# Kernel tuning notes

Hardware: AMD Instinct MI355X
Metric: run time of the kernel (lower is better)

The kernel has to match this reference:

```python
import jax, jax.numpy as jnp
import numpy as np

B, S, D = 4, 2048, 512
H, DK, DV = 8, 64, 64
EPS = 1e-6
MASK_FILL = -1e-9  # faithful to the original masked_fill value (NOT -inf)


def setup_inputs() -> dict:
    key = jax.random.key(0)
    ks = jax.random.split(key, 9)
    sc = 0.05
    return {
        "q": jax.random.normal(ks[0], (B, S, D), jnp.float32),
        "k": jax.random.normal(ks[1], (B, S, D), jnp.float32),
        "v": jax.random.normal(ks[2], (B, S, D), jnp.float32),
        "src_mask": jax.random.randint(ks[3], (B, S), 0, 2, jnp.int32),
        "Wq": jax.random.normal(ks[4], (D, H * DK), jnp.float32) * sc,
        "Wk": jax.random.normal(ks[5], (D, H * DK), jnp.float32) * sc,
        "Wv": jax.random.normal(ks[6], (D, H * DV), jnp.float32) * sc,
        "Wo": jax.random.normal(ks[7], (H * DV, D), jnp.float32) * sc,
        "gamma": jnp.ones((D,), jnp.float32),
        "beta": jnp.zeros((D,), jnp.float32),
    }


def reference(q, k, v, src_mask, Wq, Wk, Wv, Wo, gamma, beta):
    b, len_q, _ = q.shape
    residual = q
    # QKV projections -> [B, H, S, dk/dv]
    qh = (q @ Wq).reshape(b, len_q, H, DK).transpose(0, 2, 1, 3)
    kh = (k @ Wk).reshape(b, -1, H, DK).transpose(0, 2, 1, 3)
    vh = (v @ Wv).reshape(b, -1, H, DV).transpose(0, 2, 1, 3)
    # scores [B, H, S, S]
    attn = jnp.einsum('bhqd,bhkd->bhqk', qh, kh) / jnp.sqrt(jnp.float32(DK))
    # pairwise src mask: outer product of [B,S] mask, diagonal forced to 1
    sm = src_mask[:, :len_q].astype(jnp.float32)
    am = sm[:, :, None] * sm[:, None, :]               # [B, S, S]
    idx = jnp.arange(len_q)
    am = am.at[:, idx, idx].set(1.0)
    attn = jnp.where(am[:, None, :, :] == 0, MASK_FILL, attn)
    attn = jax.nn.softmax(attn, axis=-1)
    out = jnp.einsum('bhqk,bhkd->bhqd', attn, vh)      # [B, H, S, dv]
    out = out.transpose(0, 2, 1, 3).reshape(b, len_q, H * DV)
    out = out @ Wo + residual
    # LayerNorm(eps=1e-6)
    mu = jnp.mean(out, axis=-1, keepdims=True)
    var = jnp.var(out, axis=-1, keepdims=True)
    out = (out - mu) * jax.lax.rsqrt(var + EPS) * gamma + beta
    return out, attn
```

## Files before the change

### kernel.cpp

```cpp
#include <hip/hip_runtime.h>
#include <math.h>

#define B_ 4
#define S_ 2048
#define D_ 512
#define H_ 8
#define NEG_FILL (-1e-9f)

typedef __attribute__((ext_vector_type(8))) short bf16x8;
typedef __attribute__((ext_vector_type(4))) float f32x4;

#define MFMA16(A, Bm, C) __builtin_amdgcn_mfma_f32_16x16x32_bf16((A), (Bm), (C), 0, 0, 0)

__device__ __forceinline__ short f2b(float f) {
  union { float f; unsigned u; } x;
  x.f = f;
  unsigned r = x.u + 0x7fffu + ((x.u >> 16) & 1u);
  return (short)(r >> 16);
}

__global__ __launch_bounds__(256) void prep_wt(
    const float* __restrict__ Wq, const float* __restrict__ Wk,
    const float* __restrict__ Wv, const float* __restrict__ Wo,
    short* __restrict__ Wqt, short* __restrict__ Wkt,
    short* __restrict__ Wvt, short* __restrict__ Wot)
{
  const float* W; short* Wt;
  switch (blockIdx.z) {
    case 0: W = Wq; Wt = Wqt; break;
    case 1: W = Wk; Wt = Wkt; break;
    case 2: W = Wv; Wt = Wvt; break;
    default: W = Wo; Wt = Wot; break;
  }
  __shared__ float Ws[64 * 68];
  const int t = threadIdx.x;
  const int n0 = blockIdx.x * 64, k0 = blockIdx.y * 64;

  #pragma unroll
  for (int rep = 0; rep < 4; ++rep) {
    int e4 = rep * 256 + t;
    int r = e4 >> 4, c0 = (e4 & 15) * 4;
    *(float4*)&Ws[r * 68 + c0] = *(const float4*)&W[(size_t)(k0 + r) * 512 + n0 + c0];
  }
  __syncthreads();

  int rn = t >> 2;
  int kb = (t & 3) * 16;
  union { short s[8]; int4 v; } pk;
  #pragma unroll
  for (int half = 0; half < 2; ++half) {
    #pragma unroll
    for (int i = 0; i < 8; ++i)
      pk.s[i] = f2b(Ws[(kb + half * 8 + i) * 68 + rn]);
    *(int4*)&Wt[(size_t)(n0 + rn) * 512 + k0 + kb + half * 8] = pk.v;
  }
}

__global__ __launch_bounds__(256) void x2b(
    const float* __restrict__ q, const float* __restrict__ k, const float* __restrict__ v,
    short* __restrict__ qb, short* __restrict__ kb, short* __restrict__ vb)
{
  const float* X = (blockIdx.y == 0) ? q : (blockIdx.y == 1) ? k : v;
  short* Y = (blockIdx.y == 0) ? qb : (blockIdx.y == 1) ? kb : vb;
  const size_t i = ((size_t)blockIdx.x * 256 + threadIdx.x) * 8;
  float4 a = *(const float4*)&X[i];
  float4 b = *(const float4*)&X[i + 4];
  union { short s[8]; int4 v; } pk;
  pk.s[0] = f2b(a.x); pk.s[1] = f2b(a.y); pk.s[2] = f2b(a.z); pk.s[3] = f2b(a.w);
  pk.s[4] = f2b(b.x); pk.s[5] = f2b(b.y); pk.s[6] = f2b(b.z); pk.s[7] = f2b(b.w);
  *(int4*)&Y[i] = pk.v;
}

__global__ __launch_bounds__(256) void qkv_mfma(
    const short* __restrict__ qb, const short* __restrict__ kb, const short* __restrict__ vb,
    const short* __restrict__ Wqt, const short* __restrict__ Wkt, const short* __restrict__ Wvt,
    short* __restrict__ qh, short* __restrict__ kh, short* __restrict__ vt)
{
  const int z = blockIdx.z;
  const short* Xb = (z == 0) ? qb : (z == 1) ? kb : vb;
  const short* Wt = (z == 0) ? Wqt : (z == 1) ? Wkt : Wvt;

  __shared__ short Xs[64 * 72];
  __shared__ short Wsh[64 * 72];

  const int t = threadIdx.x;
  const int wave = t >> 6, lane = t & 63, quad = lane >> 4, l15 = lane & 15;
  const int tile_n = blockIdx.x * 64;
  const int tile_m = blockIdx.y * 64;

  f32x4 acc[4];
  #pragma unroll
  for (int nt = 0; nt < 4; ++nt) acc[nt] = (f32x4){0.f, 0.f, 0.f, 0.f};

  for (int k0 = 0; k0 < 512; k0 += 64) {
    __syncthreads();
    #pragma unroll
    for (int rep = 0; rep < 2; ++rep) {
      int e = rep * 256 + t;
      int row = e >> 3, c0 = (e & 7) * 8;
      *(int4*)&Xs[row * 72 + c0] = *(const int4*)&Xb[(size_t)(tile_m + row) * 512 + k0 + c0];
      *(int4*)&Wsh[row * 72 + c0] = *(const int4*)&Wt[(size_t)(tile_n + row) * 512 + k0 + c0];
    }
    __syncthreads();
    #pragma unroll
    for (int ks = 0; ks < 2; ++ks) {
      bf16x8 af = *(bf16x8*)&Xs[(wave * 16 + l15) * 72 + ks * 32 + quad * 8];
      #pragma unroll
      for (int nt = 0; nt < 4; ++nt) {
        bf16x8 bfr = *(bf16x8*)&Wsh[(nt * 16 + l15) * 72 + ks * 32 + quad * 8];
        acc[nt] = MFMA16(af, bfr, acc[nt]);
      }
    }
  }

  const int h = tile_n >> 6;
  if (z < 2) {
    short* Y = (z == 0) ? qh : kh;
    #pragma unroll
    for (int nt = 0; nt < 4; ++nt) {
      int d = nt * 16 + l15;
      #pragma unroll
      for (int r = 0; r < 4; ++r) {
        int row = tile_m + wave * 16 + quad * 4 + r;
        int b = row >> 11, s = row & (S_ - 1);
        Y[(((size_t)(b * H_ + h)) * S_ + s) * 64 + d] = f2b(acc[nt][r]);
      }
    }
  } else {
    int row0 = tile_m + wave * 16 + quad * 4;
    int b = row0 >> 11, s0 = row0 & (S_ - 1);
    #pragma unroll
    for (int nt = 0; nt < 4; ++nt) {
      int d = nt * 16 + l15;
      short4 pk = make_short4(f2b(acc[nt][0]), f2b(acc[nt][1]),
                              f2b(acc[nt][2]), f2b(acc[nt][3]));
      *(short4*)&vt[(((size_t)(b * H_ + h)) * 64 + d) * S_ + s0] = pk;
    }
  }
}

__global__ __launch_bounds__(256) void attn_mfma(
    const short* __restrict__ qh, const short* __restrict__ kh,
    const short* __restrict__ vt, const int* __restrict__ src_mask,
    float* __restrict__ attn_out, short* __restrict__ ohb)
{
  const int t = threadIdx.x;
  const int wave = t >> 6, lane = t & 63, quad = lane >> 4, l15 = lane & 15;

  const int lin = blockIdx.y * 32 + blockIdx.x;
  const int nl  = (lin & 7) * 128 + (lin >> 3);
  const int bh = nl >> 5, b = bh >> 3, h = bh & 7;
  const int q0 = (nl & 31) * 64;

  __shared__ __align__(16) short KV[4][64 * 64];
  __shared__ __align__(16) short Ps[4][16 * 72];
  __shared__ __align__(16) int smAll[S_];

  const short* __restrict__ khb = kh + (size_t)bh * S_ * 64;
  const short* __restrict__ vtb = vt + (size_t)bh * 64 * S_;

  const int sr = t >> 3, sc = t & 7;
  const int wofs0 = sr * 128 + ((sc ^ (sr & 7)) << 4);
  const int wofs1 = (sr + 32) * 128 + ((sc ^ (sr & 7)) << 4);
  const int rofs0 = ((quad ^ (l15 & 7)) << 4);
  const int rofs1 = (((4 + quad) ^ (l15 & 7)) << 4);

  const size_t qrow = (size_t)bh * S_ + q0 + wave * 16 + l15;
  const bf16x8 qf0 = *(const bf16x8*)&qh[qrow * 64 + quad * 8];
  const bf16x8 qf1 = *(const bf16x8*)&qh[qrow * 64 + 32 + quad * 8];

  int4 kreg0, kreg1, vreg0, vreg1;
  int4 mreg0 = *(const int4*)&src_mask[b * S_ + t * 4];
  int4 mreg1 = *(const int4*)&src_mask[b * S_ + (256 + t) * 4];
  kreg0 = *(const int4*)&khb[(size_t)sr * 64 + sc * 8];
  kreg1 = *(const int4*)&khb[(size_t)(sr + 32) * 64 + sc * 8];
  *(int4*)&smAll[t * 4] = mreg0;
  *(int4*)&smAll[(256 + t) * 4] = mreg1;
  *(int4*)((char*)KV[0] + wofs0) = kreg0;
  *(int4*)((char*)KV[0] + wofs1) = kreg1;
  __syncthreads();

  int rloc[4], mqr[4], qir[4];
  #pragma unroll
  for (int r = 0; r < 4; ++r) {
    rloc[r] = wave * 16 + quad * 4 + r;
    qir[r] = q0 + rloc[r];
    mqr[r] = smAll[qir[r]];
  }

  float rs[4] = {0.f, 0.f, 0.f, 0.f};
  for (int step = 0; step < 32; ++step) {
    const int kt0 = step * 64;
    const int cur = step & 1;
    if (step < 31) {
      kreg0 = *(const int4*)&khb[(size_t)(kt0 + 64 + sr) * 64 + sc * 8];
      kreg1 = *(const int4*)&khb[(size_t)(kt0 + 64 + sr + 32) * 64 + sc * 8];
    }
    const char* Kc = (const char*)KV[cur];
    #pragma unroll
    for (int nt = 0; nt < 4; ++nt) {
      bf16x8 kf0 = *(const bf16x8*)(Kc + (nt * 16 + l15) * 128 + rofs0);
      bf16x8 kf1 = *(const bf16x8*)(Kc + (nt * 16 + l15) * 128 + rofs1);
      f32x4 c = (f32x4){0.f, 0.f, 0.f, 0.f};
      c = MFMA16(qf0, kf0, c);
      c = MFMA16(qf1, kf1, c);
      int kj = kt0 + nt * 16 + l15;
      int mk = smAll[kj];
      #pragma unroll
      for (int r = 0; r < 4; ++r) {
        float ss = c[r] * 0.125f;
        bool keep = (mqr[r] & mk) || (qir[r] == kj);
        ss = keep ? ss : NEG_FILL;
        rs[r] += __expf(ss);
      }
    }
    if (step < 31) {
      *(int4*)((char*)KV[cur ^ 1] + wofs0) = kreg0;
      *(int4*)((char*)KV[cur ^ 1] + wofs1) = kreg1;
    }
    __syncthreads();
  }
  #pragma unroll
  for (int r = 0; r < 4; ++r) {
    float vsum = rs[r];
    vsum += __shfl_xor(vsum, 1);
    vsum += __shfl_xor(vsum, 2);
    vsum += __shfl_xor(vsum, 4);
    vsum += __shfl_xor(vsum, 8);
    rs[r] = 1.f / vsum;
  }

  f32x4 oacc[4];
  #pragma unroll
  for (int dt = 0; dt < 4; ++dt) oacc[dt] = (f32x4){0.f, 0.f, 0.f, 0.f};

  float* __restrict__ arow[4];
  #pragma unroll
  for (int r = 0; r < 4; ++r)
    arow[r] = attn_out + ((size_t)bh * S_ + q0 + rloc[r]) * S_;

  short* __restrict__ ps = Ps[wave];

  kreg0 = *(const int4*)&khb[(size_t)sr * 64 + sc * 8];
  kreg1 = *(const int4*)&khb[(size_t)(sr + 32) * 64 + sc * 8];
  vreg0 = *(const int4*)&vtb[(size_t)sr * S_ + sc * 8];
  vreg1 = *(const int4*)&vtb[(size_t)(sr + 32) * S_ + sc * 8];
  *(int4*)((char*)KV[0] + wofs0) = kreg0;
  *(int4*)((char*)KV[0] + wofs1) = kreg1;
  *(int4*)((char*)KV[2] + wofs0) = vreg0;
  *(int4*)((char*)KV[2] + wofs1) = vreg1;
  __syncthreads();

  for (int step = 0; step < 32; ++step) {
    const int kt0 = step * 64;
    const int cur = step & 1;
    if (step < 31) {
      kreg0 = *(const int4*)&khb[(size_t)(kt0 + 64 + sr) * 64 + sc * 8];
      kreg1 = *(const int4*)&khb[(size_t)(kt0 + 64 + sr + 32) * 64 + sc * 8];
      vreg0 = *(const int4*)&vtb[(size_t)sr * S_ + kt0 + 64 + sc * 8];
      vreg1 = *(const int4*)&vtb[(size_t)(sr + 32) * S_ + kt0 + 64 + sc * 8];
    }
    const char* Kc = (const char*)KV[cur];
    const char* Vc = (const char*)KV[2 + cur];
    #pragma unroll
    for (int nt = 0; nt < 4; ++nt) {
      bf16x8 kf0 = *(const bf16x8*)(Kc + (nt * 16 + l15) * 128 + rofs0);
      bf16x8 kf1 = *(const bf16x8*)(Kc + (nt * 16 + l15) * 128 + rofs1);
      f32x4 c = (f32x4){0.f, 0.f, 0.f, 0.f};
      c = MFMA16(qf0, kf0, c);
      c = MFMA16(qf1, kf1, c);
      int kj = kt0 + nt * 16 + l15;
      int mk = smAll[kj];
      #pragma unroll
      for (int r = 0; r < 4; ++r) {
        float ss = c[r] * 0.125f;
        bool keep = (mqr[r] & mk) || (qir[r] == kj);
        ss = keep ? ss : NEG_FILL;
        float p = __expf(ss) * rs[r];
        __builtin_nontemporal_store(p, &arow[r][kj]);
        ps[(quad * 4 + r) * 72 + nt * 16 + l15] = f2b(p);
      }
    }
    bf16x8 pf0 = *(bf16x8*)&ps[l15 * 72 + quad * 8];
    bf16x8 pf1 = *(bf16x8*)&ps[l15 * 72 + 32 + quad * 8];
    #pragma unroll
    for (int dt = 0; dt < 4; ++dt) {
      bf16x8 vf0 = *(const bf16x8*)(Vc + (dt * 16 + l15) * 128 + rofs0);
      bf16x8 vf1 = *(const bf16x8*)(Vc + (dt * 16 + l15) * 128 + rofs1);
      oacc[dt] = MFMA16(pf0, vf0, oacc[dt]);
      oacc[dt] = MFMA16(pf1, vf1, oacc[dt]);
    }
    if (step < 31) {
      *(int4*)((char*)KV[cur ^ 1] + wofs0) = kreg0;
      *(int4*)((char*)KV[cur ^ 1] + wofs1) = kreg1;
      *(int4*)((char*)KV[2 + (cur ^ 1)] + wofs0) = vreg0;
      *(int4*)((char*)KV[2 + (cur ^ 1)] + wofs1) = vreg1;
    }
    __syncthreads();
  }

  #pragma unroll
  for (int dt = 0; dt < 4; ++dt) {
    int d = h * 64 + dt * 16 + l15;
    #pragma unroll
    for (int r = 0; r < 4; ++r)
      ohb[((size_t)b * S_ + q0 + rloc[r]) * 512 + d] = f2b(oacc[dt][r]);
  }
}

__global__ __launch_bounds__(256) void out_mfma(
    const short* __restrict__ ohb, const short* __restrict__ Wot,
    const float* __restrict__ resid, float* __restrict__ out)
{
  __shared__ short Xs[64 * 72];
  __shared__ short Wsh[64 * 72];

  const int t = threadIdx.x;
  const int wave = t >> 6, lane = t & 63, quad = lane >> 4, l15 = lane & 15;
  const int tile_n = blockIdx.x * 64;
  const int tile_m = blockIdx.y * 64;

  f32x4 acc[4];
  #pragma unroll
  for (int nt = 0; nt < 4; ++nt) acc[nt] = (f32x4){0.f, 0.f, 0.f, 0.f};

  for (int k0 = 0; k0 < 512; k0 += 64) {
    __syncthreads();
    #pragma unroll
    for (int rep = 0; rep < 2; ++rep) {
      int e = rep * 256 + t;
      int row = e >> 3, c0 = (e & 7) * 8;
      *(int4*)&Xs[row * 72 + c0] = *(const int4*)&ohb[(size_t)(tile_m + row) * 512 + k0 + c0];
      *(int4*)&Wsh[row * 72 + c0] = *(const int4*)&Wot[(size_t)(tile_n + row) * 512 + k0 + c0];
    }
    __syncthreads();
    #pragma unroll
    for (int ks = 0; ks < 2; ++ks) {
      bf16x8 af = *(bf16x8*)&Xs[(wave * 16 + l15) * 72 + ks * 32 + quad * 8];
      #pragma unroll
      for (int nt = 0; nt < 4; ++nt) {
        bf16x8 bfr = *(bf16x8*)&Wsh[(nt * 16 + l15) * 72 + ks * 32 + quad * 8];
        acc[nt] = MFMA16(af, bfr, acc[nt]);
      }
    }
  }

  #pragma unroll
  for (int nt = 0; nt < 4; ++nt) {
    int c = tile_n + nt * 16 + l15;
    #pragma unroll
    for (int r = 0; r < 4; ++r) {
      size_t row = tile_m + wave * 16 + quad * 4 + r;
      out[row * 512 + c] = acc[nt][r] + resid[row * 512 + c];
    }
  }
}

__global__ __launch_bounds__(256) void ln_kernel(
    float* __restrict__ io, const float* __restrict__ gamma, const float* __restrict__ beta)
{
  const int wid  = threadIdx.x >> 6;
  const int lane = threadIdx.x & 63;
  const size_t row = (size_t)blockIdx.x * 4 + wid;
  const size_t base = row * 512 + lane * 8;

  float4 x0 = *(const float4*)&io[base];
  float4 x1 = *(const float4*)&io[base + 4];
  float xs[8] = {x0.x, x0.y, x0.z, x0.w, x1.x, x1.y, x1.z, x1.w};

  float s = 0.f, s2 = 0.f;
  #pragma unroll
  for (int i = 0; i < 8; ++i) { s += xs[i]; s2 = fmaf(xs[i], xs[i], s2); }
  #pragma unroll
  for (int m = 1; m < 64; m <<= 1) {
    s  += __shfl_xor(s, m);
    s2 += __shfl_xor(s2, m);
  }
  float mu  = s * (1.f / 512.f);
  float var = s2 * (1.f / 512.f) - mu * mu;
  float rsq = rsqrtf(var + 1e-6f);

  float4 g0 = *(const float4*)&gamma[lane * 8];
  float4 g1 = *(const float4*)&gamma[lane * 8 + 4];
  float4 b0 = *(const float4*)&beta[lane * 8];
  float4 b1 = *(const float4*)&beta[lane * 8 + 4];
  float gs[8] = {g0.x, g0.y, g0.z, g0.w, g1.x, g1.y, g1.z, g1.w};
  float bs[8] = {b0.x, b0.y, b0.z, b0.w, b1.x, b1.y, b1.z, b1.w};

  float ys[8];
  #pragma unroll
  for (int i = 0; i < 8; ++i) ys[i] = (xs[i] - mu) * rsq * gs[i] + bs[i];
  *(float4*)&io[base]     = make_float4(ys[0], ys[1], ys[2], ys[3]);
  *(float4*)&io[base + 4] = make_float4(ys[4], ys[5], ys[6], ys[7]);
}

extern "C" void kernel_launch(void* const* d_in, const int* in_sizes, int n_in,
                              void* d_out, int out_size, void* d_ws, size_t ws_size,
                              hipStream_t stream)
{
  const float* q     = (const float*)d_in[0];
  const float* k     = (const float*)d_in[1];
  const float* v     = (const float*)d_in[2];
  const int*  smask  = (const int*)d_in[3];
  const float* Wq    = (const float*)d_in[4];
  const float* Wk    = (const float*)d_in[5];
  const float* Wv    = (const float*)d_in[6];
  const float* Wo    = (const float*)d_in[7];
  const float* gamma = (const float*)d_in[8];
  const float* beta  = (const float*)d_in[9];

  float* out  = (float*)d_out;
  float* attn = out + (size_t)B_ * S_ * D_;

  short* wsS = (short*)d_ws;
  short* qh  = wsS;
  short* kh  = qh + 4194304;
  short* vt  = kh + 4194304;
  short* ohb = vt + 4194304;
  short* Wqt = ohb + 4194304;
  short* Wkt = Wqt + 262144;
  short* Wvt = Wkt + 262144;
  short* Wot = Wvt + 262144;

  short* qb = (short*)attn;
  short* kb = qb + 4194304;
  short* vb = kb + 4194304;

  prep_wt<<<dim3(8, 8, 4), 256, 0, stream>>>(Wq, Wk, Wv, Wo, Wqt, Wkt, Wvt, Wot);
  x2b<<<dim3(2048, 3), 256, 0, stream>>>(q, k, v, qb, kb, vb);
  qkv_mfma<<<dim3(8, 128, 3), 256, 0, stream>>>(qb, kb, vb, Wqt, Wkt, Wvt, qh, kh, vt);
  attn_mfma<<<dim3(32, 32), 256, 0, stream>>>(qh, kh, vt, smask, attn, ohb);
  out_mfma<<<dim3(8, 128), 256, 0, stream>>>(ohb, Wot, q, out);
  ln_kernel<<<2048, 256, 0, stream>>>(out, gamma, beta);
}
```

Before: 723.4 us.

## Cut attention LDS footprint: drop mask LDS copy, XOR-swizzle P tile, raise occupancy

Removes the 8KB shared-memory copy of the source mask and reads mask values straight from global memory, which the cache should serve. It shrinks the per-wave P staging tile from padded 72-wide rows to 64-wide rows using the same XOR swizzle as the K/V tiles. It also adds a min-blocks-per-CU hint of 4 to launch_bounds. Together these lower LDS use and register pressure so more blocks can be resident per CU, at the cost of extra global mask loads in the inner loop and possible register spills under the tighter bound.

Result: no change. 735.7 us (+1.7%).

```diff
diff --git a/kernel.cpp b/kernel.cpp
--- a/kernel.cpp
+++ b/kernel.cpp
@@ -139,7 +139,7 @@
   }
 }
 
-__global__ __launch_bounds__(256) void attn_mfma(
+__global__ __launch_bounds__(256, 4) void attn_mfma(
     const short* __restrict__ qh, const short* __restrict__ kh,
     const short* __restrict__ vt, const int* __restrict__ src_mask,
     float* __restrict__ attn_out, short* __restrict__ ohb)
@@ -153,11 +153,11 @@
   const int q0 = (nl & 31) * 64;
 
   __shared__ __align__(16) short KV[4][64 * 64];
-  __shared__ __align__(16) short Ps[4][16 * 72];
-  __shared__ __align__(16) int smAll[S_];
+  __shared__ __align__(16) short Ps[4][16 * 64];
 
   const short* __restrict__ khb = kh + (size_t)bh * S_ * 64;
   const short* __restrict__ vtb = vt + (size_t)bh * 64 * S_;
+  const int* __restrict__ smb = src_mask + b * S_;
 
   const int sr = t >> 3, sc = t & 7;
   const int wofs0 = sr * 128 + ((sc ^ (sr & 7)) << 4);
@@ -170,23 +170,19 @@
   const bf16x8 qf1 = *(const bf16x8*)&qh[qrow * 64 + 32 + quad * 8];
 
   int4 kreg0, kreg1, vreg0, vreg1;
-  int4 mreg0 = *(const int4*)&src_mask[b * S_ + t * 4];
-  int4 mreg1 = *(const int4*)&src_mask[b * S_ + (256 + t) * 4];
   kreg0 = *(const int4*)&khb[(size_t)sr * 64 + sc * 8];
   kreg1 = *(const int4*)&khb[(size_t)(sr + 32) * 64 + sc * 8];
-  *(int4*)&smAll[t * 4] = mreg0;
-  *(int4*)&smAll[(256 + t) * 4] = mreg1;
   *(int4*)((char*)KV[0] + wofs0) = kreg0;
   *(int4*)((char*)KV[0] + wofs1) = kreg1;
-  __syncthreads();
 
   int rloc[4], mqr[4], qir[4];
   #pragma unroll
   for (int r = 0; r < 4; ++r) {
     rloc[r] = wave * 16 + quad * 4 + r;
     qir[r] = q0 + rloc[r];
-    mqr[r] = smAll[qir[r]];
-  }
+    mqr[r] = smb[qir[r]];
+  }
+  __syncthreads();
 
   float rs[4] = {0.f, 0.f, 0.f, 0.f};
   for (int step = 0; step < 32; ++step) {
@@ -196,6 +192,9 @@
       kreg0 = *(const int4*)&khb[(size_t)(kt0 + 64 + sr) * 64 + sc * 8];
       kreg1 = *(const int4*)&khb[(size_t)(kt0 + 64 + sr + 32) * 64 + sc * 8];
     }
+    int mk_[4];
+    #pragma unroll
+    for (int nt = 0; nt < 4; ++nt) mk_[nt] = smb[kt0 + nt * 16 + l15];
     const char* Kc = (const char*)KV[cur];
     #pragma unroll
     for (int nt = 0; nt < 4; ++nt) {
@@ -205,11 +204,10 @@
       c = MFMA16(qf0, kf0, c);
       c = MFMA16(qf1, kf1, c);
       int kj = kt0 + nt * 16 + l15;
-      int mk = smAll[kj];
       #pragma unroll
       for (int r = 0; r < 4; ++r) {
         float ss = c[r] * 0.125f;
-        bool keep = (mqr[r] & mk) || (qir[r] == kj);
+        bool keep = (mqr[r] & mk_[nt]) || (qir[r] == kj);
         ss = keep ? ss : NEG_FILL;
         rs[r] += __expf(ss);
       }
@@ -240,6 +238,14 @@
     arow[r] = attn_out + ((size_t)bh * S_ + q0 + rloc[r]) * S_;
 
   short* __restrict__ ps = Ps[wave];
+  const int hb = l15 >> 3;
+  int pbase[4], prx[4];
+  #pragma unroll
+  for (int r = 0; r < 4; ++r) {
+    int rowb = quad * 4 + r;
+    pbase[r] = rowb * 128 + (l15 & 7) * 2;
+    prx[r] = rowb & 7;
+  }
 
   kreg0 = *(const int4*)&khb[(size_t)sr * 64 + sc * 8];
   kreg1 = *(const int4*)&khb[(size_t)(sr + 32) * 64 + sc * 8];
@@ -260,6 +266,9 @@
       vreg0 = *(const int4*)&vtb[(size_t)sr * S_ + kt0 + 64 + sc * 8];
       vreg1 = *(const int4*)&vtb[(size_t)(sr + 32) * S_ + kt0 + 64 + sc * 8];
     }
+    int mk_[4];
+    #pragma unroll
+    for (int nt = 0; nt < 4; ++nt) mk_[nt] = smb[kt0 + nt * 16 + l15];
     const char* Kc = (const char*)KV[cur];
     const char* Vc = (const char*)KV[2 + cur];
     #pragma unroll
@@ -270,19 +279,19 @@
       c = MFMA16(qf0, kf0, c);
       c = MFMA16(qf1, kf1, c);
       int kj = kt0 + nt * 16 + l15;
-      int mk = smAll[kj];
+      const int sb = ((nt << 1) | hb);
       #pragma unroll
       for (int r = 0; r < 4; ++r) {
         float ss = c[r] * 0.125f;
-        bool keep = (mqr[r] & mk) || (qir[r] == kj);
+        bool keep = (mqr[r] & mk_[nt]) || (qir[r] == kj);
         ss = keep ? ss : NEG_FILL;
         float p = __expf(ss) * rs[r];
         __builtin_nontemporal_store(p, &arow[r][kj]);
-        ps[(quad * 4 + r) * 72 + nt * 16 + l15] = f2b(p);
+        *(short*)((char*)ps + pbase[r] + ((sb ^ prx[r]) << 4)) = f2b(p);
       }
     }
-    bf16x8 pf0 = *(bf16x8*)&ps[l15 * 72 + quad * 8];
-    bf16x8 pf1 = *(bf16x8*)&ps[l15 * 72 + 32 + quad * 8];
+    bf16x8 pf0 = *(bf16x8*)((char*)ps + l15 * 128 + rofs0);
+    bf16x8 pf1 = *(bf16x8*)((char*)ps + l15 * 128 + rofs1);
     #pragma unroll
     for (int dt = 0; dt < 4; ++dt) {
       bf16x8 vf0 = *(const bf16x8*)(Vc + (dt * 16 + l15) * 128 + rofs0);
```
